# Kernel optimization log

Measured on AMD Instinct MI355X. Metric: run time of the kernel, lower is better.

Reference implementation:

```python
import jax, jax.numpy as jnp
import numpy as np

# Module config (matches init_kwargs)
T = 4096          # max_seq_length == runtime seq len
L = 1024          # local_size
BQ = 16           # block_q (q bucket size in flash loop)
BK = 128          # block_k (k bucket size in flash loop)
C = 128           # query chunk size used for the banded jax formulation (multiple of BQ, == BK)
NC = T // C       # number of query chunks
W = L + C         # key window width per query chunk: [chunk_start - L, chunk_start + C)
HEAD_DIM = 64
NUM_HEAD = 16
SCALE = 1.0 / float(np.sqrt(HEAD_DIM))


def _build_mask():
    # Reproduces the flash path's sparsity: a (q,k) pair is kept iff
    #   j <= i  (element-level causal) AND
    #   k_block_start(j) >= q_block_start(i) - local_size  (block skip rule)
    # where q_block_start = (i//BQ)*BQ, k_block_start = (j//BK)*BK.
    i_loc = np.arange(C)                      # query offset inside chunk
    j_rel = np.arange(W) - L                  # key offset relative to chunk start
    causal = j_rel[None, :] <= i_loc[:, None]
    kb = (j_rel // BK) * BK                   # floor-div works for negatives
    qb = (i_loc // BQ) * BQ
    local_ok = kb[None, :] >= qb[:, None] - L
    static = causal & local_ok                # [C, W], chunk-independent
    starts = np.arange(NC) * C
    valid = (starts[:, None] + j_rel[None, :]) >= 0   # mask out left padding
    return jnp.asarray(static[None, :, :] & valid[:, None, :])  # [NC, C, W]

MASK = _build_mask()


def setup_inputs() -> dict:
    key = jax.random.key(0)
    k1, k2, k3 = jax.random.split(key, 3)
    B = 2
    E = NUM_HEAD * HEAD_DIM
    q = jax.random.normal(k1, (T, B, E), jnp.float32)
    k = jax.random.normal(k2, (T, B, E), jnp.float32)
    v = jax.random.normal(k3, (T, B, E), jnp.float32)
    padding_mask = jnp.zeros((B, T), bool)     # unused by module's forward
    attention_mask = jnp.zeros((B, T), bool)   # unused by module's forward
    return {"q": q, "k": k, "v": v, "padding_mask": padding_mask, "attention_mask": attention_mask}


def _attend(qh, kh, vh):
    # qh/kh/vh: [BH, T, D]; banded local+causal attention
    BH, _, D = qh.shape
    qr = (qh * SCALE).reshape(BH, NC, C, D)
    kp = jnp.pad(kh, ((0, 0), (L, 0), (0, 0)))
    vp = jnp.pad(vh, ((0, 0), (L, 0), (0, 0)))
    # window gather: chunk c covers padded indices [c*C, c*C + W)
    idx = jnp.arange(NC)[:, None] * C + jnp.arange(W)[None, :]   # [NC, W]
    kw = kp[:, idx]   # [BH, NC, W, D]
    vw = vp[:, idx]   # [BH, NC, W, D]
    s = jnp.einsum('bcid,bcjd->bcij', qr, kw)      # [BH, NC, C, W]
    s = jnp.where(MASK, s, -jnp.inf)
    p = jax.nn.softmax(s, axis=-1)                 # every row has a valid (diagonal) entry
    o = jnp.einsum('bcij,bcjd->bcid', p, vw)
    return o.reshape(BH, T, D)


def reference(q, k, v, padding_mask, attention_mask):
    Tq, B, E = q.shape
    # (T, B, H*D) -> (B*H, T, D), matching view(T, B*H, D).transpose(0,1)
    qh = q.reshape(Tq, B * NUM_HEAD, HEAD_DIM).transpose(1, 0, 2)
    kh = k.reshape(Tq, B * NUM_HEAD, HEAD_DIM).transpose(1, 0, 2)
    vh = v.reshape(Tq, B * NUM_HEAD, HEAD_DIM).transpose(1, 0, 2)
    o = _attend(qh, kh, vh)                        # [B*H, T, D]
    # out.transpose(0,1).view(T, B, H*D)
    return o.transpose(1, 0, 2).reshape(Tq, B, E)
```

## Files before the change

kernel.cpp:

```cpp
#include <hip/hip_runtime.h>
#include <hip/hip_bf16.h>

typedef float f32x16 __attribute__((ext_vector_type(16)));
typedef short bf16x8 __attribute__((ext_vector_type(8)));

#define SCALE2 0.1803368801111242f

#define EXP2(x) __builtin_amdgcn_exp2f(x)

static __device__ __forceinline__ unsigned int pk2(float a, float b) {
  unsigned short lo = __builtin_bit_cast(unsigned short, __float2bfloat16(a));
  unsigned short hi = __builtin_bit_cast(unsigned short, __float2bfloat16(b));
  return (unsigned int)lo | ((unsigned int)hi << 16);
}

#define GLDS16(g, l) __builtin_amdgcn_global_load_lds(                      \
    (const __attribute__((address_space(1))) unsigned int*)(g),             \
    (__attribute__((address_space(3))) unsigned int*)(l), 16, 0, 0)

extern "C" __global__ __launch_bounds__(256)
void prep_k(const float* __restrict__ k, char* __restrict__ ks)
{
  const int idx = blockIdx.x * 256 + threadIdx.x;
  const int fb  = idx * 8;
  const int t   = fb >> 11;
  const int rem = fb & 2047;
  const int bh  = rem >> 6;
  const int d0  = rem & 63;
  const float* sp = k + fb;
  const float4 f0 = *(const float4*)sp;
  const float4 f1 = *(const float4*)(sp + 4);
  uint4 u;
  u.x = pk2(f0.x, f0.y); u.y = pk2(f0.z, f0.w);
  u.z = pk2(f1.x, f1.y); u.w = pk2(f1.z, f1.w);
  const size_t ob = (size_t)bh * 524288 + (size_t)t * 128 + ((d0 * 2) ^ ((t & 7) << 4));
  *(uint4*)(ks + ob) = u;
}

extern "C" __global__ __launch_bounds__(256)
void prep_v(const float* __restrict__ v, char* __restrict__ vts)
{
  __shared__ float Lt[64 * 65];
  const int bh   = blockIdx.x >> 6;
  const int tile = blockIdx.x & 63;
  const int t0   = tile * 64;
  const int b = bh >> 4, h = bh & 15;
  const float* vp = v + (size_t)t0 * 2048 + b * 1024 + h * 64;
  const int tid = threadIdx.x;
  const int dd = tid & 63, tl = tid >> 6;
  #pragma unroll
  for (int p2 = 0; p2 < 16; ++p2) {
    const int t_loc = p2 * 4 + tl;
    Lt[dd * 65 + t_loc] = vp[(size_t)t_loc * 2048 + dd];
  }
  __syncthreads();
  const int d = tid >> 2, tg = tid & 3;
  float a[16];
  #pragma unroll
  for (int j = 0; j < 16; ++j) a[j] = Lt[d * 65 + tg * 16 + j];
  uint4 u0, u1;
  u0.x = pk2(a[0], a[1]);  u0.y = pk2(a[2], a[3]);
  u0.z = pk2(a[4], a[5]);  u0.w = pk2(a[6], a[7]);
  u1.x = pk2(a[8], a[9]);  u1.y = pk2(a[10], a[11]);
  u1.z = pk2(a[12], a[13]); u1.w = pk2(a[14], a[15]);
  const size_t ob = (size_t)bh * 524288 + (size_t)d * 8192;
  const int off0 = t0 * 2 + tg * 32;
  const int swz = (d & 7) << 4;
  *(uint4*)(vts + ob + ((off0) ^ swz))      = u0;
  *(uint4*)(vts + ob + ((off0 + 16) ^ swz)) = u1;
}

extern "C" __global__ __launch_bounds__(512, 4)
void sparse_attn8(const float* __restrict__ qg, const char* __restrict__ ks,
                  const char* __restrict__ vts, float* __restrict__ og)
{
  __shared__ __align__(16) char lds[32768];

  const int w    = blockIdx.x;
  const int work = (w & 7) * 64 + (w >> 3);
  const int cp   = work & 15;
  const int bh   = work >> 4;

  const int tid = threadIdx.x;
  const int wq  = tid >> 6;
  const int g   = wq >> 2;
  const int wv  = wq & 3;
  const int ln  = tid & 63;
  const int l31 = ln & 31;
  const int hi  = ln >> 5;

  const int c  = cp * 2 + g;
  const int ql = wv * 32 + l31;
  const int qt = c * 128 + ql;
  const size_t hb = (size_t)bh * 524288;
  const int b = bh >> 4, h = bh & 15;

  bf16x8 qf[4];
  {
    const float* qp = qg + (size_t)qt * 2048 + b * 1024 + h * 64;
    #pragma unroll
    for (int kd = 0; kd < 4; ++kd) {
      const int d0 = kd * 16 + hi * 8;
      const float4 f0 = *(const float4*)(qp + d0);
      const float4 f1 = *(const float4*)(qp + d0 + 4);
      uint4 u;
      u.x = pk2(f0.x * SCALE2, f0.y * SCALE2);
      u.y = pk2(f0.z * SCALE2, f0.w * SCALE2);
      u.z = pk2(f1.x * SCALE2, f1.y * SCALE2);
      u.w = pk2(f1.z * SCALE2, f1.w * SCALE2);
      qf[kd] = __builtin_bit_cast(bf16x8, u);
    }
  }

  f32x16 ot[2];
  #pragma unroll
  for (int i = 0; i < 2; ++i)
    #pragma unroll
    for (int r = 0; r < 16; ++r) ot[i][r] = 0.f;

  float lsum = 0.f;

  const int nr0 = (cp >= 4) ? 0 : (16 - 4 * cp);

  const char* kga = ks  + hb + (size_t)((4 * cp - 16 + nr0) * 64) * 128 + tid * 16;
  const char* vga = vts + hb + (size_t)(tid >> 3) * 8192
                    + (size_t)((4 * cp - 16 + nr0) * 64) * 2 + (tid & 7) * 16;

  auto STAGE = [&](int p) {
    char* kl = lds + p * 16384 + wq * 1024;
    char* vl = lds + p * 16384 + 8192 + wq * 1024;
    GLDS16(kga, kl);
    GLDS16(vga, vl);
  };

  STAGE(0);
  kga += 8192; vga += 128;
  __syncthreads();

  int p = 0;
  for (int nr = nr0; nr <= 19; ++nr) {
    if (nr < 19) {
      STAGE(p ^ 1);
      kga += 8192; vga += 128;
    }

    const int n = nr - 2 * g;
    const bool act = (n >= 0) && (n <= 17)
                  && !((n <= 1) && (wv > 0))
                  && !((n == 17) && (wv < 2));
    if (act) {
      const char* Kl = lds + p * 16384;
      const char* Vt = lds + p * 16384 + 8192;

      f32x16 st[2];
      #pragma unroll
      for (int mt = 0; mt < 2; ++mt)
        #pragma unroll
        for (int r = 0; r < 16; ++r) st[mt][r] = 0.f;

      __builtin_amdgcn_s_setprio(1);
      #pragma unroll
      for (int kd = 0; kd < 4; ++kd) {
        #pragma unroll
        for (int mt = 0; mt < 2; ++mt) {
          const int key  = mt * 32 + l31;
          const int boff = (key * 128 + kd * 32 + hi * 16) ^ ((key & 7) << 4);
          const bf16x8 kf = *(const bf16x8*)(Kl + boff);
          st[mt] = __builtin_amdgcn_mfma_f32_32x32x16_bf16(kf, qf[kd], st[mt], 0, 0, 0);
        }
      }
      __builtin_amdgcn_s_setprio(0);

      if (n >= 16 && wv * 32 < (n - 16) * 64 + 64) {
        const int base = (n - 16) * 64;
        #pragma unroll
        for (int mt = 0; mt < 2; ++mt)
          #pragma unroll
          for (int r = 0; r < 16; ++r) {
            const int kl2 = base + mt * 32 + (r & 3) + 8 * (r >> 2) + 4 * hi;
            if (kl2 > ql) st[mt][r] = -1e30f;
          }
      }

      const bool dead = (n <= 1) && (l31 >= 16);
      if (!dead) {
        #pragma unroll
        for (int mt = 0; mt < 2; ++mt)
          #pragma unroll
          for (int r = 0; r < 16; ++r)
            st[mt][r] = EXP2(st[mt][r]);
      } else {
        #pragma unroll
        for (int mt = 0; mt < 2; ++mt)
          #pragma unroll
          for (int r = 0; r < 16; ++r) st[mt][r] = 0.f;
      }

      #pragma unroll
      for (int mt = 0; mt < 2; ++mt) {
        #pragma unroll
        for (int s = 0; s < 2; ++s) {
          const unsigned int X0 = pk2(st[mt][s * 8 + 0], st[mt][s * 8 + 1]);
          const unsigned int X1 = pk2(st[mt][s * 8 + 2], st[mt][s * 8 + 3]);
          const unsigned int Y0 = pk2(st[mt][s * 8 + 4], st[mt][s * 8 + 5]);
          const unsigned int Y1 = pk2(st[mt][s * 8 + 6], st[mt][s * 8 + 7]);
          const unsigned int s0 = hi ? X0 : Y0;
          const unsigned int s1 = hi ? X1 : Y1;
          const unsigned int r0 = (unsigned int)__shfl_xor((int)s0, 32);
          const unsigned int r1 = (unsigned int)__shfl_xor((int)s1, 32);
          uint4 u;
          if (hi == 0) { u.x = X0; u.y = X1; u.z = r0; u.w = r1; }
          else         { u.x = r0; u.y = r1; u.z = Y0; u.w = Y1; }
          const bf16x8 pf = __builtin_bit_cast(bf16x8, u);
          const int ks2 = mt * 2 + s;
          __builtin_amdgcn_s_setprio(1);
          #pragma unroll
          for (int dt = 0; dt < 2; ++dt) {
            const int d    = dt * 32 + l31;
            const int boff = d * 128 + ((ks2 * 32 + hi * 16) ^ ((d & 7) << 4));
            const bf16x8 vf = *(const bf16x8*)(Vt + boff);
            ot[dt] = __builtin_amdgcn_mfma_f32_32x32x16_bf16(vf, pf, ot[dt], 0, 0, 0);
          }
          __builtin_amdgcn_s_setprio(0);
        }
      }

      if (!dead) {
        float t[16];
        #pragma unroll
        for (int r = 0; r < 16; ++r) t[r] = st[0][r] + st[1][r];
        #pragma unroll
        for (int s2 = 8; s2 >= 1; s2 >>= 1)
          #pragma unroll
          for (int r = 0; r < 8; ++r)
            if (r < s2) t[r] += t[r + s2];
        lsum += t[0];
      }
    }

    __syncthreads();
    p ^= 1;
  }

  float lt = lsum + __shfl_xor(lsum, 32);
  const float rl = 1.0f / lt;

  float* op = og + (size_t)qt * 2048 + b * 1024 + h * 64;
  #pragma unroll
  for (int dt = 0; dt < 2; ++dt)
    #pragma unroll
    for (int g2 = 0; g2 < 4; ++g2) {
      float4 o4;
      o4.x = ot[dt][g2 * 4 + 0] * rl;
      o4.y = ot[dt][g2 * 4 + 1] * rl;
      o4.z = ot[dt][g2 * 4 + 2] * rl;
      o4.w = ot[dt][g2 * 4 + 3] * rl;
      *(float4*)(op + dt * 32 + g2 * 8 + hi * 4) = o4;
    }
}

extern "C" __global__ __launch_bounds__(256)
void sparse_attn_v1(const float* __restrict__ qg, const float* __restrict__ kg,
                    const float* __restrict__ vg, float* __restrict__ og)
{
  __shared__ unsigned short Kl[128 * 64];
  __shared__ unsigned short Vt[64 * 128];

  const int bx  = blockIdx.x;
  const int c   = bx & 31;
  const int bh  = bx >> 5;
  const int b   = bh >> 4;
  const int h   = bh & 15;

  const int tid = threadIdx.x;
  const int wv  = tid >> 6;
  const int ln  = tid & 63;
  const int l31 = ln & 31;
  const int hi  = ln >> 5;

  const int ql = wv * 32 + l31;
  const int qt = c * 128 + ql;
  const size_t hoff = (size_t)b * 1024 + (size_t)h * 64;

  bf16x8 qf[4];
  {
    const float* qp = qg + (size_t)qt * 2048 + hoff;
    #pragma unroll
    for (int kd = 0; kd < 4; ++kd) {
      const int d0 = kd * 16 + hi * 8;
      const float4 f0 = *(const float4*)(qp + d0);
      const float4 f1 = *(const float4*)(qp + d0 + 4);
      uint4 u;
      u.x = pk2(f0.x * SCALE2, f0.y * SCALE2);
      u.y = pk2(f0.z * SCALE2, f0.w * SCALE2);
      u.z = pk2(f1.x * SCALE2, f1.y * SCALE2);
      u.w = pk2(f1.z * SCALE2, f1.w * SCALE2);
      qf[kd] = __builtin_bit_cast(bf16x8, u);
    }
  }

  f32x16 ot[2];
  #pragma unroll
  for (int i = 0; i < 2; ++i)
    #pragma unroll
    for (int r = 0; r < 16; ++r) ot[i][r] = 0.f;

  float m_run = -1e30f, l_run = 0.f;

  const int n0 = (c >= 8) ? 0 : (8 - c);
  for (int n = n0; n <= 8; ++n) {
    const int ka = (c - 8 + n) * 128;

    __syncthreads();
    {
      const int key = tid & 127;
      const int dh  = tid >> 7;
      const float* kp = kg + (size_t)(ka + key) * 2048 + hoff + dh * 32;
      #pragma unroll
      for (int u2 = 0; u2 < 4; ++u2) {
        const float4 f0 = *(const float4*)(kp + u2 * 8);
        const float4 f1 = *(const float4*)(kp + u2 * 8 + 4);
        uint4 w2;
        w2.x = pk2(f0.x, f0.y); w2.y = pk2(f0.z, f0.w);
        w2.z = pk2(f1.x, f1.y); w2.w = pk2(f1.z, f1.w);
        const int boff = (key * 128 + dh * 64 + u2 * 16) ^ ((key & 7) << 4);
        *(uint4*)((char*)Kl + boff) = w2;
      }
    }
    {
      const int kp2 = tid & 63;
      const int dq  = tid >> 6;
      const float* vp = vg + (size_t)(ka + kp2 * 2) * 2048 + hoff + dq * 16;
      float va[16], vb[16];
      #pragma unroll
      for (int u2 = 0; u2 < 4; ++u2) {
        *(float4*)(va + u2 * 4) = *(const float4*)(vp + u2 * 4);
        *(float4*)(vb + u2 * 4) = *(const float4*)(vp + 2048 + u2 * 4);
      }
      #pragma unroll
      for (int j = 0; j < 16; ++j) {
        const int d = dq * 16 + j;
        const unsigned int wrd = pk2(va[j], vb[j]);
        const int boff = d * 256 + ((kp2 * 4) ^ ((d & 7) << 4));
        *(unsigned int*)((char*)Vt + boff) = wrd;
      }
    }
    __syncthreads();

    if (n == 0 && wv > 0) continue;

    f32x16 st[4];
    #pragma unroll
    for (int mt = 0; mt < 4; ++mt)
      #pragma unroll
      for (int r = 0; r < 16; ++r) st[mt][r] = 0.f;

    #pragma unroll
    for (int kd = 0; kd < 4; ++kd) {
      #pragma unroll
      for (int mt = 0; mt < 4; ++mt) {
        const int key  = mt * 32 + l31;
        const int boff = (key * 128 + kd * 32 + hi * 16) ^ ((key & 7) << 4);
        const bf16x8 kf = *(const bf16x8*)((const char*)Kl + boff);
        st[mt] = __builtin_amdgcn_mfma_f32_32x32x16_bf16(kf, qf[kd], st[mt], 0, 0, 0);
      }
    }

    if (n == 8) {
      #pragma unroll
      for (int mt = 0; mt < 4; ++mt)
        #pragma unroll
        for (int r = 0; r < 16; ++r) {
          const int kl = mt * 32 + (r & 3) + 8 * (r >> 2) + 4 * hi;
          if (kl > ql) st[mt][r] = -1e30f;
        }
    }

    const bool dead = (n == 0) && (l31 >= 16);
    float alpha = 1.f;
    if (!dead) {
      float pm = -1e30f;
      #pragma unroll
      for (int mt = 0; mt < 4; ++mt)
        #pragma unroll
        for (int r = 0; r < 16; ++r) pm = fmaxf(pm, st[mt][r]);
      pm = fmaxf(pm, __shfl_xor(pm, 32));
      const float m_new = fmaxf(m_run, pm);
      alpha = exp2f(m_run - m_new);
      float ps = 0.f;
      #pragma unroll
      for (int mt = 0; mt < 4; ++mt)
        #pragma unroll
        for (int r = 0; r < 16; ++r) {
          const float pv = exp2f(st[mt][r] - m_new);
          st[mt][r] = pv;
          ps += pv;
        }
      ps += __shfl_xor(ps, 32);
      l_run = l_run * alpha + ps;
      m_run = m_new;
    } else {
      #pragma unroll
      for (int mt = 0; mt < 4; ++mt)
        #pragma unroll
        for (int r = 0; r < 16; ++r) st[mt][r] = 0.f;
    }
    ot[0] *= alpha;
    ot[1] *= alpha;

    #pragma unroll
    for (int mt = 0; mt < 4; ++mt) {
      #pragma unroll
      for (int s = 0; s < 2; ++s) {
        const unsigned int X0 = pk2(st[mt][s * 8 + 0], st[mt][s * 8 + 1]);
        const unsigned int X1 = pk2(st[mt][s * 8 + 2], st[mt][s * 8 + 3]);
        const unsigned int Y0 = pk2(st[mt][s * 8 + 4], st[mt][s * 8 + 5]);
        const unsigned int Y1 = pk2(st[mt][s * 8 + 6], st[mt][s * 8 + 7]);
        const unsigned int s0 = hi ? X0 : Y0;
        const unsigned int s1 = hi ? X1 : Y1;
        const unsigned int r0 = (unsigned int)__shfl_xor((int)s0, 32);
        const unsigned int r1 = (unsigned int)__shfl_xor((int)s1, 32);
        uint4 u;
        if (hi == 0) { u.x = X0; u.y = X1; u.z = r0; u.w = r1; }
        else         { u.x = r0; u.y = r1; u.z = Y0; u.w = Y1; }
        const bf16x8 pf = __builtin_bit_cast(bf16x8, u);
        const int ks = mt * 2 + s;
        #pragma unroll
        for (int dt = 0; dt < 2; ++dt) {
          const int d    = dt * 32 + l31;
          const int boff = (d * 256 + ks * 32 + hi * 16) ^ ((d & 7) << 4);
          const bf16x8 vf = *(const bf16x8*)((const char*)Vt + boff);
          ot[dt] = __builtin_amdgcn_mfma_f32_32x32x16_bf16(vf, pf, ot[dt], 0, 0, 0);
        }
      }
    }
  }

  const float rl = 1.0f / l_run;
  float* op = og + (size_t)qt * 2048 + hoff;
  #pragma unroll
  for (int dt = 0; dt < 2; ++dt)
    #pragma unroll
    for (int g = 0; g < 4; ++g) {
      float4 o4;
      o4.x = ot[dt][g * 4 + 0] * rl;
      o4.y = ot[dt][g * 4 + 1] * rl;
      o4.z = ot[dt][g * 4 + 2] * rl;
      o4.w = ot[dt][g * 4 + 3] * rl;
      *(float4*)(op + dt * 32 + g * 8 + hi * 4) = o4;
    }
}

extern "C" void kernel_launch(void* const* d_in, const int* in_sizes, int n_in,
                              void* d_out, int out_size, void* d_ws, size_t ws_size,
                              hipStream_t stream) {
  const float* q = (const float*)d_in[0];
  const float* k = (const float*)d_in[1];
  const float* v = (const float*)d_in[2];
  float* o = (float*)d_out;

  const size_t NEED = 2ull * 16777216ull;
  if (ws_size >= NEED) {
    char* kss = (char*)d_ws;
    char* vts = kss + 16777216;
    hipLaunchKernelGGL(prep_k, dim3(4096), dim3(256), 0, stream, k, kss);
    hipLaunchKernelGGL(prep_v, dim3(2048), dim3(256), 0, stream, v, vts);
    hipLaunchKernelGGL(sparse_attn8, dim3(512), dim3(512), 0, stream,
                       q, (const char*)kss, (const char*)vts, o);
  } else {
    hipLaunchKernelGGL(sparse_attn_v1, dim3(1024), dim3(256), 0, stream, q, k, v, o);
  }
}
```

Before: 97.56 us.

## Fuse K/V prep kernels and load V fragments directly from global in MFMA layout

Merges the K and V preprocessing into a single launch and rewrites V into a fragment-ordered layout so each lane can load its MFMA B-operands straight from global memory into registers. V staging through LDS is dropped. The attention kernel shrinks from 512-thread blocks covering two query chunks to 256-thread blocks covering one, halving LDS per block and doubling the grid. This removes a launch and LDS traffic for V, but adds per-iteration global loads of V with no prefetch and loses the K tile sharing between two chunks.

```diff
diff --git a/kernel.cpp b/kernel.cpp
--- a/kernel.cpp
+++ b/kernel.cpp
@@ -19,77 +19,73 @@
     (__attribute__((address_space(3))) unsigned int*)(l), 16, 0, 0)
 
 extern "C" __global__ __launch_bounds__(256)
-void prep_k(const float* __restrict__ k, char* __restrict__ ks)
-{
-  const int idx = blockIdx.x * 256 + threadIdx.x;
-  const int fb  = idx * 8;
-  const int t   = fb >> 11;
-  const int rem = fb & 2047;
-  const int bh  = rem >> 6;
-  const int d0  = rem & 63;
-  const float* sp = k + fb;
-  const float4 f0 = *(const float4*)sp;
-  const float4 f1 = *(const float4*)(sp + 4);
-  uint4 u;
-  u.x = pk2(f0.x, f0.y); u.y = pk2(f0.z, f0.w);
-  u.z = pk2(f1.x, f1.y); u.w = pk2(f1.z, f1.w);
-  const size_t ob = (size_t)bh * 524288 + (size_t)t * 128 + ((d0 * 2) ^ ((t & 7) << 4));
-  *(uint4*)(ks + ob) = u;
-}
-
-extern "C" __global__ __launch_bounds__(256)
-void prep_v(const float* __restrict__ v, char* __restrict__ vts)
+void prep_kv(const float* __restrict__ k, const float* __restrict__ v,
+             char* __restrict__ ks, char* __restrict__ vf)
 {
   __shared__ float Lt[64 * 65];
-  const int bh   = blockIdx.x >> 6;
-  const int tile = blockIdx.x & 63;
-  const int t0   = tile * 64;
-  const int b = bh >> 4, h = bh & 15;
-  const float* vp = v + (size_t)t0 * 2048 + b * 1024 + h * 64;
   const int tid = threadIdx.x;
-  const int dd = tid & 63, tl = tid >> 6;
-  #pragma unroll
-  for (int p2 = 0; p2 < 16; ++p2) {
-    const int t_loc = p2 * 4 + tl;
-    Lt[dd * 65 + t_loc] = vp[(size_t)t_loc * 2048 + dd];
-  }
-  __syncthreads();
-  const int d = tid >> 2, tg = tid & 3;
-  float a[16];
-  #pragma unroll
-  for (int j = 0; j < 16; ++j) a[j] = Lt[d * 65 + tg * 16 + j];
-  uint4 u0, u1;
-  u0.x = pk2(a[0], a[1]);  u0.y = pk2(a[2], a[3]);
-  u0.z = pk2(a[4], a[5]);  u0.w = pk2(a[6], a[7]);
-  u1.x = pk2(a[8], a[9]);  u1.y = pk2(a[10], a[11]);
-  u1.z = pk2(a[12], a[13]); u1.w = pk2(a[14], a[15]);
-  const size_t ob = (size_t)bh * 524288 + (size_t)d * 8192;
-  const int off0 = t0 * 2 + tg * 32;
-  const int swz = (d & 7) << 4;
-  *(uint4*)(vts + ob + ((off0) ^ swz))      = u0;
-  *(uint4*)(vts + ob + ((off0 + 16) ^ swz)) = u1;
+  if (blockIdx.x < 4096) {
+    const int idx = blockIdx.x * 256 + tid;
+    const int fb  = idx * 8;
+    const int t   = fb >> 11;
+    const int rem = fb & 2047;
+    const int bh  = rem >> 6;
+    const int d0  = rem & 63;
+    const float* sp = k + fb;
+    const float4 f0 = *(const float4*)sp;
+    const float4 f1 = *(const float4*)(sp + 4);
+    uint4 u;
+    u.x = pk2(f0.x, f0.y); u.y = pk2(f0.z, f0.w);
+    u.z = pk2(f1.x, f1.y); u.w = pk2(f1.z, f1.w);
+    const size_t ob = (size_t)bh * 524288 + (size_t)t * 128 + ((d0 * 2) ^ ((t & 7) << 4));
+    *(uint4*)(ks + ob) = u;
+  } else {
+    const int bx = blockIdx.x - 4096;
+    const int bh = bx >> 6;
+    const int kb = bx & 63;
+    const int t0 = kb * 64;
+    const int b = bh >> 4, h = bh & 15;
+    const float* vp = v + (size_t)t0 * 2048 + b * 1024 + h * 64;
+    const int dd = tid & 63, tl = tid >> 6;
+    #pragma unroll
+    for (int p2 = 0; p2 < 16; ++p2) {
+      const int t_loc = p2 * 4 + tl;
+      Lt[dd * 65 + t_loc] = vp[(size_t)t_loc * 2048 + dd];
+    }
+    __syncthreads();
+    const int d = tid >> 2, tg = tid & 3;
+    float a[16];
+    #pragma unroll
+    for (int j = 0; j < 16; ++j) a[j] = Lt[d * 65 + tg * 16 + j];
+    uint4 u0, u1;
+    u0.x = pk2(a[0], a[1]);   u0.y = pk2(a[2], a[3]);
+    u0.z = pk2(a[4], a[5]);   u0.w = pk2(a[6], a[7]);
+    u1.x = pk2(a[8], a[9]);   u1.y = pk2(a[10], a[11]);
+    u1.z = pk2(a[12], a[13]); u1.w = pk2(a[14], a[15]);
+    const size_t base = (size_t)bh * 524288 + (size_t)kb * 8192
+                      + tg * 2048 + (d >> 5) * 1024 + (d & 31) * 16;
+    *(uint4*)(vf + base)       = u0;
+    *(uint4*)(vf + base + 512) = u1;
+  }
 }
 
-extern "C" __global__ __launch_bounds__(512, 4)
-void sparse_attn8(const float* __restrict__ qg, const char* __restrict__ ks,
-                  const char* __restrict__ vts, float* __restrict__ og)
+extern "C" __global__ __launch_bounds__(256, 4)
+void sparse_attn9(const float* __restrict__ qg, const char* __restrict__ ksw,
+                  const char* __restrict__ vfr, float* __restrict__ og)
 {
-  __shared__ __align__(16) char lds[32768];
+  __shared__ __align__(16) char lds[16384];
 
   const int w    = blockIdx.x;
-  const int work = (w & 7) * 64 + (w >> 3);
-  const int cp   = work & 15;
-  const int bh   = work >> 4;
+  const int work = (w & 7) * 128 + (w >> 3);
+  const int c    = work & 31;
+  const int bh   = work >> 5;
 
   const int tid = threadIdx.x;
-  const int wq  = tid >> 6;
-  const int g   = wq >> 2;
-  const int wv  = wq & 3;
+  const int wv  = tid >> 6;
   const int ln  = tid & 63;
   const int l31 = ln & 31;
   const int hi  = ln >> 5;
 
-  const int c  = cp * 2 + g;
   const int ql = wv * 32 + l31;
   const int qt = c * 128 + ql;
   const size_t hb = (size_t)bh * 524288;
@@ -120,37 +116,37 @@
 
   float lsum = 0.f;
 
-  const int nr0 = (cp >= 4) ? 0 : (16 - 4 * cp);
-
-  const char* kga = ks  + hb + (size_t)((4 * cp - 16 + nr0) * 64) * 128 + tid * 16;
-  const char* vga = vts + hb + (size_t)(tid >> 3) * 8192
-                    + (size_t)((4 * cp - 16 + nr0) * 64) * 2 + (tid & 7) * 16;
+  const int n0 = (c >= 8) ? 0 : (16 - 2 * c);
+
+  const char* kga = ksw + hb + (size_t)((2 * c - 16 + n0) * 64) * 128
+                    + wv * 2048 + ln * 16;
+  const char* vgb = vfr + hb + (size_t)(2 * c - 16 + n0) * 8192 + ln * 16;
 
   auto STAGE = [&](int p) {
-    char* kl = lds + p * 16384 + wq * 1024;
-    char* vl = lds + p * 16384 + 8192 + wq * 1024;
-    GLDS16(kga, kl);
-    GLDS16(vga, vl);
+    char* kl = lds + p * 8192 + wv * 2048;
+    GLDS16(kga,        kl);
+    GLDS16(kga + 1024, kl + 1024);
   };
 
   STAGE(0);
-  kga += 8192; vga += 128;
+  kga += 8192;
   __syncthreads();
 
   int p = 0;
-  for (int nr = nr0; nr <= 19; ++nr) {
-    if (nr < 19) {
+  for (int n = n0; n <= 17; ++n) {
+    if (n < 17) {
       STAGE(p ^ 1);
-      kga += 8192; vga += 128;
-    }
-
-    const int n = nr - 2 * g;
-    const bool act = (n >= 0) && (n <= 17)
-                  && !((n <= 1) && (wv > 0))
-                  && !((n == 17) && (wv < 2));
+      kga += 8192;
+    }
+
+    const bool act = !((n <= 1) && (wv > 0)) && !((n == 17) && (wv < 2));
     if (act) {
-      const char* Kl = lds + p * 16384;
-      const char* Vt = lds + p * 16384 + 8192;
+      bf16x8 vr[8];
+      #pragma unroll
+      for (int i = 0; i < 8; ++i)
+        vr[i] = *(const bf16x8*)(vgb + (i >> 1) * 2048 + (i & 1) * 1024);
+
+      const char* Kl = lds + p * 8192;
 
       f32x16 st[2];
       #pragma unroll
@@ -215,12 +211,9 @@
           const int ks2 = mt * 2 + s;
           __builtin_amdgcn_s_setprio(1);
           #pragma unroll
-          for (int dt = 0; dt < 2; ++dt) {
-            const int d    = dt * 32 + l31;
-            const int boff = d * 128 + ((ks2 * 32 + hi * 16) ^ ((d & 7) << 4));
-            const bf16x8 vf = *(const bf16x8*)(Vt + boff);
-            ot[dt] = __builtin_amdgcn_mfma_f32_32x32x16_bf16(vf, pf, ot[dt], 0, 0, 0);
-          }
+          for (int dt = 0; dt < 2; ++dt)
+            ot[dt] = __builtin_amdgcn_mfma_f32_32x32x16_bf16(vr[ks2 * 2 + dt], pf,
+                                                             ot[dt], 0, 0, 0);
           __builtin_amdgcn_s_setprio(0);
         }
       }
@@ -238,6 +231,7 @@
       }
     }
 
+    vgb += 8192;
     __syncthreads();
     p ^= 1;
   }
@@ -462,11 +456,10 @@
   const size_t NEED = 2ull * 16777216ull;
   if (ws_size >= NEED) {
     char* kss = (char*)d_ws;
-    char* vts = kss + 16777216;
-    hipLaunchKernelGGL(prep_k, dim3(4096), dim3(256), 0, stream, k, kss);
-    hipLaunchKernelGGL(prep_v, dim3(2048), dim3(256), 0, stream, v, vts);
-    hipLaunchKernelGGL(sparse_attn8, dim3(512), dim3(512), 0, stream,
-                       q, (const char*)kss, (const char*)vts, o);
+    char* vff = kss + 16777216;
+    hipLaunchKernelGGL(prep_kv, dim3(6144), dim3(256), 0, stream, k, v, kss, vff);
+    hipLaunchKernelGGL(sparse_attn9, dim3(1024), dim3(256), 0, stream,
+                       q, (const char*)kss, (const char*)vff, o);
   } else {
     hipLaunchKernelGGL(sparse_attn_v1, dim3(1024), dim3(256), 0, stream, q, k, v, o);
   }
```

Result: slower. 148.7 us (+52.4%).

## Merge K/V prep kernels and split attention to one chunk per block

Applied to the files above, without the earlier changes.

Combines the K and V bf16 preprocessing kernels into a single launch, removing one kernel launch. The attention kernel now runs 256-thread blocks that each handle one query chunk, instead of 512-thread blocks sharing a staged K/V stream across two chunks. This drops the skewed loop and trades cross-chunk K/V reuse in LDS for more independent blocks. V is stored in a permuted element order so the P fragment can be packed directly without the cross-lane shuffle.

```diff
diff --git a/kernel.cpp b/kernel.cpp
--- a/kernel.cpp
+++ b/kernel.cpp
@@ -19,77 +19,74 @@
     (__attribute__((address_space(3))) unsigned int*)(l), 16, 0, 0)
 
 extern "C" __global__ __launch_bounds__(256)
-void prep_k(const float* __restrict__ k, char* __restrict__ ks)
-{
-  const int idx = blockIdx.x * 256 + threadIdx.x;
-  const int fb  = idx * 8;
-  const int t   = fb >> 11;
-  const int rem = fb & 2047;
-  const int bh  = rem >> 6;
-  const int d0  = rem & 63;
-  const float* sp = k + fb;
-  const float4 f0 = *(const float4*)sp;
-  const float4 f1 = *(const float4*)(sp + 4);
-  uint4 u;
-  u.x = pk2(f0.x, f0.y); u.y = pk2(f0.z, f0.w);
-  u.z = pk2(f1.x, f1.y); u.w = pk2(f1.z, f1.w);
-  const size_t ob = (size_t)bh * 524288 + (size_t)t * 128 + ((d0 * 2) ^ ((t & 7) << 4));
-  *(uint4*)(ks + ob) = u;
-}
-
-extern "C" __global__ __launch_bounds__(256)
-void prep_v(const float* __restrict__ v, char* __restrict__ vts)
+void prep_kv(const float* __restrict__ k, const float* __restrict__ v,
+             char* __restrict__ ks, char* __restrict__ vts)
 {
   __shared__ float Lt[64 * 65];
-  const int bh   = blockIdx.x >> 6;
-  const int tile = blockIdx.x & 63;
-  const int t0   = tile * 64;
-  const int b = bh >> 4, h = bh & 15;
-  const float* vp = v + (size_t)t0 * 2048 + b * 1024 + h * 64;
   const int tid = threadIdx.x;
-  const int dd = tid & 63, tl = tid >> 6;
-  #pragma unroll
-  for (int p2 = 0; p2 < 16; ++p2) {
-    const int t_loc = p2 * 4 + tl;
-    Lt[dd * 65 + t_loc] = vp[(size_t)t_loc * 2048 + dd];
-  }
-  __syncthreads();
-  const int d = tid >> 2, tg = tid & 3;
-  float a[16];
-  #pragma unroll
-  for (int j = 0; j < 16; ++j) a[j] = Lt[d * 65 + tg * 16 + j];
-  uint4 u0, u1;
-  u0.x = pk2(a[0], a[1]);  u0.y = pk2(a[2], a[3]);
-  u0.z = pk2(a[4], a[5]);  u0.w = pk2(a[6], a[7]);
-  u1.x = pk2(a[8], a[9]);  u1.y = pk2(a[10], a[11]);
-  u1.z = pk2(a[12], a[13]); u1.w = pk2(a[14], a[15]);
-  const size_t ob = (size_t)bh * 524288 + (size_t)d * 8192;
-  const int off0 = t0 * 2 + tg * 32;
-  const int swz = (d & 7) << 4;
-  *(uint4*)(vts + ob + ((off0) ^ swz))      = u0;
-  *(uint4*)(vts + ob + ((off0 + 16) ^ swz)) = u1;
+  if (blockIdx.x < 4096) {
+    const int idx = blockIdx.x * 256 + tid;
+    const int fb  = idx * 8;
+    const int t   = fb >> 11;
+    const int rem = fb & 2047;
+    const int bh  = rem >> 6;
+    const int d0  = rem & 63;
+    const float* sp = k + fb;
+    const float4 f0 = *(const float4*)sp;
+    const float4 f1 = *(const float4*)(sp + 4);
+    uint4 u;
+    u.x = pk2(f0.x, f0.y); u.y = pk2(f0.z, f0.w);
+    u.z = pk2(f1.x, f1.y); u.w = pk2(f1.z, f1.w);
+    const size_t ob = (size_t)bh * 524288 + (size_t)t * 128 + ((d0 * 2) ^ ((t & 7) << 4));
+    *(uint4*)(ks + ob) = u;
+  } else {
+    const int bx   = blockIdx.x - 4096;
+    const int bh   = bx >> 6;
+    const int tile = bx & 63;
+    const int t0   = tile * 64;
+    const int b = bh >> 4, h = bh & 15;
+    const float* vp = v + (size_t)t0 * 2048 + b * 1024 + h * 64;
+    const int dd = tid & 63, tl = tid >> 6;
+    #pragma unroll
+    for (int p2 = 0; p2 < 16; ++p2) {
+      const int t_loc = p2 * 4 + tl;
+      Lt[dd * 65 + t_loc] = vp[(size_t)t_loc * 2048 + dd];
+    }
+    __syncthreads();
+    const int d = tid >> 2, tg = tid & 3;
+    float a[16];
+    #pragma unroll
+    for (int j = 0; j < 16; ++j) a[j] = Lt[d * 65 + tg * 16 + j];
+    uint4 u0, u1;
+    u0.x = pk2(a[0], a[1]);   u0.y = pk2(a[2], a[3]);
+    u0.z = pk2(a[8], a[9]);   u0.w = pk2(a[10], a[11]);
+    u1.x = pk2(a[4], a[5]);   u1.y = pk2(a[6], a[7]);
+    u1.z = pk2(a[12], a[13]); u1.w = pk2(a[14], a[15]);
+    const size_t ob = (size_t)bh * 524288 + (size_t)d * 8192;
+    const int off0 = t0 * 2 + tg * 32;
+    const int swz = (d & 7) << 4;
+    *(uint4*)(vts + ob + ((off0) ^ swz))      = u0;
+    *(uint4*)(vts + ob + ((off0 + 16) ^ swz)) = u1;
+  }
 }
 
-extern "C" __global__ __launch_bounds__(512, 4)
-void sparse_attn8(const float* __restrict__ qg, const char* __restrict__ ks,
-                  const char* __restrict__ vts, float* __restrict__ og)
+extern "C" __global__ __launch_bounds__(256, 4)
+void sparse_attn10(const float* __restrict__ qg, const char* __restrict__ ksw,
+                   const char* __restrict__ vts, float* __restrict__ og)
 {
   __shared__ __align__(16) char lds[32768];
 
   const int w    = blockIdx.x;
-  const int work = (w & 7) * 64 + (w >> 3);
-  const int cp   = work & 15;
-  const int bh   = work >> 4;
+  const int work = (w & 7) * 128 + (w >> 3);
+  const int c    = work & 31;
+  const int bh   = work >> 5;
 
   const int tid = threadIdx.x;
-  const int wq  = tid >> 6;
-  const int g   = wq >> 2;
-  const int wv  = wq & 3;
+  const int wv  = tid >> 6;
   const int ln  = tid & 63;
   const int l31 = ln & 31;
   const int hi  = ln >> 5;
 
-  const int c  = cp * 2 + g;
   const int ql = wv * 32 + l31;
   const int qt = c * 128 + ql;
   const size_t hb = (size_t)bh * 524288;
@@ -120,17 +117,20 @@
 
   float lsum = 0.f;
 
-  const int nr0 = (cp >= 4) ? 0 : (16 - 4 * cp);
-
-  const char* kga = ks  + hb + (size_t)((4 * cp - 16 + nr0) * 64) * 128 + tid * 16;
-  const char* vga = vts + hb + (size_t)(tid >> 3) * 8192
-                    + (size_t)((4 * cp - 16 + nr0) * 64) * 2 + (tid & 7) * 16;
+  const int n0 = (c >= 8) ? 0 : (16 - 2 * c);
+
+  const char* kga = ksw + hb + (size_t)((2 * c - 16 + n0) * 64) * 128
+                    + wv * 2048 + ln * 16;
+  const char* vga = vts + hb + (size_t)(wv * 16 + (ln >> 3)) * 8192
+                    + (size_t)((2 * c - 16 + n0) * 64) * 2 + (ln & 7) * 16;
 
   auto STAGE = [&](int p) {
-    char* kl = lds + p * 16384 + wq * 1024;
-    char* vl = lds + p * 16384 + 8192 + wq * 1024;
-    GLDS16(kga, kl);
-    GLDS16(vga, vl);
+    char* kl = lds + p * 16384 + wv * 2048;
+    char* vl = lds + p * 16384 + 8192 + wv * 2048;
+    GLDS16(kga,            kl);
+    GLDS16(kga + 1024,     kl + 1024);
+    GLDS16(vga,            vl);
+    GLDS16(vga + 8 * 8192, vl + 1024);
   };
 
   STAGE(0);
@@ -138,17 +138,14 @@
   __syncthreads();
 
   int p = 0;
-  for (int nr = nr0; nr <= 19; ++nr) {
-    if (nr < 19) {
+  for (int n = n0; n <= 17; ++n) {
+    if (n < 17) {
       STAGE(p ^ 1);
       kga += 8192; vga += 128;
     }
 
-    const int n = nr - 2 * g;
-    const bool act = (n >= 0) && (n <= 17)
-                  && !((n <= 1) && (wv > 0))
-                  && !((n == 17) && (wv < 2));
-    if (act) {
+    const bool skip = ((n <= 1) && (wv > 0)) || ((n == 17) && (wv < 2));
+    if (!skip) {
       const char* Kl = lds + p * 16384;
       const char* Vt = lds + p * 16384 + 8192;
 
@@ -200,17 +197,11 @@
       for (int mt = 0; mt < 2; ++mt) {
         #pragma unroll
         for (int s = 0; s < 2; ++s) {
-          const unsigned int X0 = pk2(st[mt][s * 8 + 0], st[mt][s * 8 + 1]);
-          const unsigned int X1 = pk2(st[mt][s * 8 + 2], st[mt][s * 8 + 3]);
-          const unsigned int Y0 = pk2(st[mt][s * 8 + 4], st[mt][s * 8 + 5]);
-          const unsigned int Y1 = pk2(st[mt][s * 8 + 6], st[mt][s * 8 + 7]);
-          const unsigned int s0 = hi ? X0 : Y0;
-          const unsigned int s1 = hi ? X1 : Y1;
-          const unsigned int r0 = (unsigned int)__shfl_xor((int)s0, 32);
-          const unsigned int r1 = (unsigned int)__shfl_xor((int)s1, 32);
           uint4 u;
-          if (hi == 0) { u.x = X0; u.y = X1; u.z = r0; u.w = r1; }
-          else         { u.x = r0; u.y = r1; u.z = Y0; u.w = Y1; }
+          u.x = pk2(st[mt][s * 8 + 0], st[mt][s * 8 + 1]);
+          u.y = pk2(st[mt][s * 8 + 2], st[mt][s * 8 + 3]);
+          u.z = pk2(st[mt][s * 8 + 4], st[mt][s * 8 + 5]);
+          u.w = pk2(st[mt][s * 8 + 6], st[mt][s * 8 + 7]);
           const bf16x8 pf = __builtin_bit_cast(bf16x8, u);
           const int ks2 = mt * 2 + s;
           __builtin_amdgcn_s_setprio(1);
@@ -463,9 +454,8 @@
   if (ws_size >= NEED) {
     char* kss = (char*)d_ws;
     char* vts = kss + 16777216;
-    hipLaunchKernelGGL(prep_k, dim3(4096), dim3(256), 0, stream, k, kss);
-    hipLaunchKernelGGL(prep_v, dim3(2048), dim3(256), 0, stream, v, vts);
-    hipLaunchKernelGGL(sparse_attn8, dim3(512), dim3(512), 0, stream,
+    hipLaunchKernelGGL(prep_kv, dim3(6144), dim3(256), 0, stream, k, v, kss, vts);
+    hipLaunchKernelGGL(sparse_attn10, dim3(1024), dim3(256), 0, stream,
                        q, (const char*)kss, (const char*)vts, o);
   } else {
     hipLaunchKernelGGL(sparse_attn_v1, dim3(1024), dim3(256), 0, stream, q, k, v, o);
```

New measurement: 79.10 us, median of 2. 1.23x faster.
